# Kernel tuning notes

Measured on AMD Instinct MI355X. Metric: run time of the kernel, lower is better.

Reference implementation:

```python
import jax, jax.numpy as jnp
import numpy as np

T, D, F, E, K, R = 16384, 1024, 2048, 8, 2, 16
LORA_SCALING = 2.0


def setup_inputs() -> dict:
    key = jax.random.key(0)
    ks = jax.random.split(key, 9)
    s = 0.02
    return {
        "hidden_states": jax.random.normal(ks[0], (T, D), jnp.float32),
        "gate_weight": jax.random.normal(ks[1], (E, D), jnp.float32) * s,
        "gate_lora_delta": jax.random.normal(ks[2], (E, D), jnp.float32) * s,
        "gate_up_proj": jax.random.normal(ks[3], (E, D, 2 * F), jnp.float32) * s,
        "down_proj": jax.random.normal(ks[4], (E, F, D), jnp.float32) * s,
        "gu_lora_A": jax.random.normal(ks[5], (E, R, D), jnp.float32) * s,
        "gu_lora_B": jax.random.normal(ks[6], (E, 2 * F, R), jnp.float32) * s,
        "dn_lora_A": jax.random.normal(ks[7], (E, R, F), jnp.float32) * s,
        "dn_lora_B": jax.random.normal(ks[8], (E, D, R), jnp.float32) * s,
    }


def reference(hidden_states, gate_weight, gate_lora_delta, gate_up_proj,
              down_proj, gu_lora_A, gu_lora_B, dn_lora_A, dn_lora_B):
    x = hidden_states  # [T, D]
    # --- softmax top-k routing (base gate weight + LoRA delta) ---
    logits = x @ gate_weight.T + x @ gate_lora_delta.T            # [T, E]
    probs = jax.nn.softmax(logits.astype(jnp.float32), axis=-1)   # fp32 softmax
    topk_w, topk_idx = jax.lax.top_k(probs, K)                    # [T, K]
    topk_w = topk_w / jnp.sum(topk_w, axis=-1, keepdims=True)     # norm_topk_prob
    # dense combine weights [T, E]: 0 for unselected experts
    combine = jnp.zeros((x.shape[0], E), jnp.float32)
    combine = combine.at[jnp.arange(x.shape[0])[:, None], topk_idx].set(topk_w)
    # --- per-expert gated MLP with LoRA deltas, masked combine ---
    out = jnp.zeros_like(x, dtype=jnp.float32)
    for e in range(E):  # fixed small expert count
        gu = x @ gate_up_proj[e] + LORA_SCALING * ((x @ gu_lora_A[e].T) @ gu_lora_B[e].T)  # [T, 2F]
        gate, up = jnp.split(gu, 2, axis=-1)
        h = jax.nn.silu(gate) * up                                                        # [T, F]
        y = h @ down_proj[e] + LORA_SCALING * ((h @ dn_lora_A[e].T) @ dn_lora_B[e].T)     # [T, D]
        out = out + combine[:, e:e + 1] * y
    return out.astype(hidden_states.dtype)
```

## Files before the change

kernel.cpp:

```cpp
#include <hip/hip_runtime.h>
#include <stdint.h>

#define T_TOK 16384
#define DH    1024
#define FF    2048
#define NE    8
#define NC    4096
#define PADROWS 34816
#define BK    32

typedef __attribute__((ext_vector_type(8))) __bf16 bf16x8;
typedef __attribute__((ext_vector_type(4))) float  f32x4;

__device__ __forceinline__ float bf2f(unsigned short s) {
  unsigned int u = ((unsigned int)s) << 16;
  return __builtin_bit_cast(float, u);
}
__device__ __forceinline__ unsigned short f2bf(float f) {
  unsigned int u = __builtin_bit_cast(unsigned int, f);
  u += 0x7fffu + ((u >> 16) & 1u);
  return (unsigned short)(u >> 16);
}

__device__ __forceinline__ void gload_lds16(const void* g, void* l) {
  __builtin_amdgcn_global_load_lds(
      (__attribute__((address_space(1))) void*)(uintptr_t)g,
      (__attribute__((address_space(3))) void*)(uint32_t)(uintptr_t)l,
      16, 0, 0);
}

__device__ __forceinline__ int origc_gu(int c) {
  int g = c >> 5, wi = c & 31;
  return ((wi >> 4) << 11) | (g * 16 + (wi & 15));
}

__global__ __launch_bounds__(256) void fold_gu_kernel(
    const float* __restrict__ Wg, const float* __restrict__ A,
    const float* __restrict__ B, unsigned short* __restrict__ Wf)
{
  const int e = blockIdx.x, d0 = blockIdx.y * 64, c0 = blockIdx.z * 64;
  __shared__ float tile[64][65];
  __shared__ float Al[16][64];
  __shared__ float Bl[64][17];
  const int tid = threadIdx.x;
  {
    int r = tid >> 4, dc = (tid & 15) * 4;
    float4 v = *(const float4*)&A[((size_t)e * 16 + r) * DH + d0 + dc];
    Al[r][dc] = v.x; Al[r][dc + 1] = v.y; Al[r][dc + 2] = v.z; Al[r][dc + 3] = v.w;
  }
  {
    int c = tid >> 2, rr = (tid & 3) * 4;
    float4 v = *(const float4*)&B[((size_t)e * NC + origc_gu(c0 + c)) * 16 + rr];
    Bl[c][rr] = v.x; Bl[c][rr + 1] = v.y; Bl[c][rr + 2] = v.z; Bl[c][rr + 3] = v.w;
  }
  __syncthreads();
  const int d = tid >> 2;
  const int cq0 = (tid & 3) * 4;
  float areg[16];
#pragma unroll
  for (int r = 0; r < 16; r++) areg[r] = Al[r][d];
#pragma unroll
  for (int p = 0; p < 4; p++) {
    const int cq = p * 16 + cq0;
    float4 v = *(const float4*)&Wg[((size_t)e * DH + d0 + d) * NC + origc_gu(c0 + cq)];
    float s0 = 0.f, s1 = 0.f, s2 = 0.f, s3 = 0.f;
#pragma unroll
    for (int r = 0; r < 16; r++) {
      float a = areg[r];
      s0 += a * Bl[cq][r];     s1 += a * Bl[cq + 1][r];
      s2 += a * Bl[cq + 2][r]; s3 += a * Bl[cq + 3][r];
    }
    tile[d][cq]     = v.x + 2.f * s0; tile[d][cq + 1] = v.y + 2.f * s1;
    tile[d][cq + 2] = v.z + 2.f * s2; tile[d][cq + 3] = v.w + 2.f * s3;
  }
  __syncthreads();
#pragma unroll
  for (int p = 0; p < 2; p++) {
    int flat = p * 256 + tid;
    int c = flat >> 3, dch = (flat & 7) * 8;
    unsigned short u[8];
#pragma unroll
    for (int j = 0; j < 8; j++) u[j] = f2bf(tile[dch + j][c]);
    *(uint4*)&Wf[((size_t)e * NC + c0 + c) * DH + d0 + dch] = *(uint4*)u;
  }
}

__global__ __launch_bounds__(256) void fold_dn_kernel(
    const float* __restrict__ Wd, const float* __restrict__ A,
    const float* __restrict__ B, unsigned short* __restrict__ Wf)
{
  const int e = blockIdx.x, f0 = blockIdx.y * 64, d0 = blockIdx.z * 64;
  __shared__ float tile[64][65];
  __shared__ float Al[16][64];
  __shared__ float Bl[64][17];
  const int tid = threadIdx.x;
  {
    int r = tid >> 4, fc = (tid & 15) * 4;
    float4 v = *(const float4*)&A[((size_t)e * 16 + r) * FF + f0 + fc];
    Al[r][fc] = v.x; Al[r][fc + 1] = v.y; Al[r][fc + 2] = v.z; Al[r][fc + 3] = v.w;
  }
  {
    int d = tid >> 2, rr = (tid & 3) * 4;
    float4 v = *(const float4*)&B[((size_t)e * DH + d0 + d) * 16 + rr];
    Bl[d][rr] = v.x; Bl[d][rr + 1] = v.y; Bl[d][rr + 2] = v.z; Bl[d][rr + 3] = v.w;
  }
  __syncthreads();
  const int f = tid >> 2;
  const int dq0 = (tid & 3) * 4;
  float areg[16];
#pragma unroll
  for (int r = 0; r < 16; r++) areg[r] = Al[r][f];
#pragma unroll
  for (int p = 0; p < 4; p++) {
    const int dq = p * 16 + dq0;
    float4 v = *(const float4*)&Wd[((size_t)e * FF + f0 + f) * DH + d0 + dq];
    float s0 = 0.f, s1 = 0.f, s2 = 0.f, s3 = 0.f;
#pragma unroll
    for (int r = 0; r < 16; r++) {
      float a = areg[r];
      s0 += a * Bl[dq][r];     s1 += a * Bl[dq + 1][r];
      s2 += a * Bl[dq + 2][r]; s3 += a * Bl[dq + 3][r];
    }
    tile[f][dq]     = v.x + 2.f * s0; tile[f][dq + 1] = v.y + 2.f * s1;
    tile[f][dq + 2] = v.z + 2.f * s2; tile[f][dq + 3] = v.w + 2.f * s3;
  }
  __syncthreads();
#pragma unroll
  for (int p = 0; p < 2; p++) {
    int flat = p * 256 + tid;
    int d = flat >> 3, fch = (flat & 7) * 8;
    unsigned short u[8];
#pragma unroll
    for (int j = 0; j < 8; j++) u[j] = f2bf(tile[fch + j][d]);
    *(uint4*)&Wf[((size_t)e * DH + d0 + d) * FF + f0 + fch] = *(uint4*)u;
  }
}

__global__ __launch_bounds__(256) void route_kernel(
    const float* __restrict__ X,
    const float* __restrict__ GW,
    const float* __restrict__ GLD,
    unsigned short* __restrict__ Xbf,
    int* __restrict__ tokE, float* __restrict__ tokW, int* __restrict__ counts)
{
  __shared__ float gc[NE * DH];
  __shared__ int bc[NE];
  const int tid = threadIdx.x;
  if (tid < NE) bc[tid] = 0;
  for (int i = tid; i < NE * DH; i += 256) gc[i] = GW[i] + GLD[i];
  __syncthreads();
  const int w = tid >> 6, lane = tid & 63;
  for (int it = 0; it < 8; it++) {
    const int t = blockIdx.x * 32 + w * 8 + it;
    float s[NE];
#pragma unroll
    for (int e = 0; e < NE; e++) s[e] = 0.f;
#pragma unroll
    for (int i = 0; i < 8; i++) {
      const int base = 2 * lane + 128 * i;
      const float2 xv = *(const float2*)&X[(size_t)t * DH + base];
      *(unsigned*)&Xbf[(size_t)t * DH + base] =
          (unsigned)f2bf(xv.x) | ((unsigned)f2bf(xv.y) << 16);
#pragma unroll
      for (int e = 0; e < NE; e++) {
        float2 g2 = *(const float2*)&gc[e * DH + base];
        s[e] += xv.x * g2.x + xv.y * g2.y;
      }
    }
#pragma unroll
    for (int e = 0; e < NE; e++) {
#pragma unroll
      for (int off = 32; off > 0; off >>= 1) s[e] += __shfl_xor(s[e], off);
    }
    int e1 = 0; float l1 = s[0];
#pragma unroll
    for (int e = 1; e < NE; e++) { if (s[e] > l1) { l1 = s[e]; e1 = e; } }
    int e2i = 0; float l2 = -3.4e38f;
#pragma unroll
    for (int e = 0; e < NE; e++) { if (e != e1 && s[e] > l2) { l2 = s[e]; e2i = e; } }
    float r = __expf(l2 - l1);
    float w0 = 1.f / (1.f + r);
    if (lane == 0) {
      tokE[2 * t] = e1; tokE[2 * t + 1] = e2i;
      tokW[2 * t] = w0; tokW[2 * t + 1] = 1.f - w0;
      atomicAdd(&bc[e1], 1); atomicAdd(&bc[e2i], 1);
    }
  }
  __syncthreads();
  if (tid < NE) atomicAdd(&counts[tid], bc[tid]);
}

__global__ void offs_kernel(const int* __restrict__ counts, int* __restrict__ offs) {
  if (threadIdx.x == 0) {
    int run = 0;
#pragma unroll
    for (int e = 0; e < NE; e++) { offs[e] = run; run += (counts[e] + 255) & ~255; }
    offs[NE] = run;
  }
}

__global__ void scatter_kernel(const int* __restrict__ tokE,
                               const int* __restrict__ offs,
                               int* __restrict__ cursor,
                               int* __restrict__ posTok,
                               int* __restrict__ posOf)
{
  const int t = blockIdx.x * 256 + threadIdx.x;
  const int lane = threadIdx.x & 63;
#pragma unroll
  for (int k = 0; k < 2; k++) {
    const int e = tokE[2 * t + k];
    int p = 0;
#pragma unroll
    for (int ei = 0; ei < NE; ei++) {
      unsigned long long mask = __ballot(e == ei);
      if (mask) {
        int leader = __ffsll((unsigned long long)mask) - 1;
        int base = 0;
        if (lane == leader) base = atomicAdd(&cursor[ei], (int)__popcll(mask));
        base = __shfl(base, leader);
        if (e == ei)
          p = offs[ei] + base + (int)__popcll(mask & ((1ull << lane) - 1ull));
      }
    }
    if (p < 0) p = 0;
    if (p >= PADROWS) p = PADROWS - 1;
    posTok[p] = t;
    posOf[2 * t + k] = p;
  }
}


#define STAGE_A(s) { unsigned short* d_ = (unsigned short*)&lds[(s) & 3][0][w * 512]; \
  gload_lds16(gA0 + (size_t)(s) * BK, d_); gload_lds16(gA1 + (size_t)(s) * BK, d_ + 4096); }
#define STAGE_B(s) { unsigned short* d_ = (unsigned short*)&lds[(s) & 3][1][w * 512]; \
  gload_lds16(gB0 + (size_t)(s) * BK, d_); gload_lds16(gB1 + (size_t)(s) * BK, d_ + 4096); }

#define PHASE_MFMA(ACCROW, AV)                                              \
  __builtin_amdgcn_s_barrier();                                             \
  __builtin_amdgcn_s_setprio(1);                                            \
  _Pragma("unroll")                                                         \
  for (int mi = 0; mi < 4; mi++)                                            \
    _Pragma("unroll")                                                       \
    for (int ni = 0; ni < 4; ni++)                                          \
      acc[(ACCROW) + mi][ni] = __builtin_amdgcn_mfma_f32_16x16x32_bf16(     \
          AV[mi], b[ni], acc[(ACCROW) + mi][ni], 0, 0, 0);                  \
  __builtin_amdgcn_s_setprio(0);                                            \
  __builtin_amdgcn_s_barrier();

__global__ __launch_bounds__(512, 2) void gemm1_kernel(
    const unsigned short* __restrict__ Xbf,
    const unsigned short* __restrict__ Wgu,
    const int* __restrict__ posTok,
    const int* __restrict__ offs,
    unsigned short* __restrict__ H)
{
  __shared__ __align__(16) unsigned short lds[4][2][8192];
  const int NT = DH / BK;
  const int n0 = blockIdx.x * 256;
  const int row0 = blockIdx.y * 256;
  if (row0 >= offs[NE]) return;
  int e = 0;
#pragma unroll
  for (int i = 1; i < NE; i++) e += (row0 >= offs[i]) ? 1 : 0;
  const unsigned short* Wb = Wgu + (size_t)e * NC * DH;

  const int tid = threadIdx.x;
  const int lane = tid & 63;
  const int w = tid >> 6;
  const int wm = w >> 2, wn = w & 3;
  const int l15 = lane & 15, quad = lane >> 4;

  const int srow = tid >> 2;
  const int sch  = (tid & 3) ^ ((srow >> 1) & 3);
  int t0 = posTok[row0 + srow];       if (t0 < 0) t0 = 0;
  int t1 = posTok[row0 + 128 + srow]; if (t1 < 0) t1 = 0;
  const unsigned short* gA0 = Xbf + (size_t)t0 * DH + sch * 8;
  const unsigned short* gA1 = Xbf + (size_t)t1 * DH + sch * 8;
  const unsigned short* gB0 = Wb + (size_t)(n0 + srow) * DH + sch * 8;
  const unsigned short* gB1 = Wb + (size_t)(n0 + 128 + srow) * DH + sch * 8;

  const int slot  = quad ^ ((l15 >> 1) & 3);
  const int aBase = (wm * 128 + l15) * 32 + slot * 8;
  const int bBase = (wn * 64 + l15) * 32 + slot * 8;

  f32x4 acc[8][4];
#pragma unroll
  for (int mi = 0; mi < 8; mi++)
#pragma unroll
    for (int ni = 0; ni < 4; ni++) acc[mi][ni] = (f32x4){0.f, 0.f, 0.f, 0.f};

  STAGE_A(0); STAGE_B(0);
  STAGE_A(1); STAGE_B(1);
  STAGE_A(2); STAGE_B(2);
  asm volatile("s_waitcnt vmcnt(8)" ::: "memory");
  __builtin_amdgcn_s_barrier();

  for (int kt = 0; kt < NT; ++kt) {
    const unsigned short* LA = &lds[kt & 3][0][0];
    const unsigned short* LB = &lds[kt & 3][1][0];
    bf16x8 a[4], b[4];
#pragma unroll
    for (int i = 0; i < 4; i++) a[i] = *(const bf16x8*)&LA[aBase + i * 512];
#pragma unroll
    for (int i = 0; i < 4; i++) b[i] = *(const bf16x8*)&LB[bBase + i * 512];
    if (kt + 3 < NT) STAGE_A(kt + 3);
    PHASE_MFMA(0, a)
    bf16x8 a2[4];
#pragma unroll
    for (int i = 0; i < 4; i++) a2[i] = *(const bf16x8*)&LA[aBase + (4 + i) * 512];
    if (kt + 3 < NT) STAGE_B(kt + 3);
    if (kt + 3 < NT)       { asm volatile("s_waitcnt vmcnt(8)" ::: "memory"); }
    else if (kt + 3 == NT) { asm volatile("s_waitcnt vmcnt(4)" ::: "memory"); }
    else if (kt + 1 < NT)  { asm volatile("s_waitcnt vmcnt(0)" ::: "memory"); }
    PHASE_MFMA(4, a2)
  }

  const int rowb = row0 + wm * 128;
#pragma unroll
  for (int mi = 0; mi < 8; mi++) {
#pragma unroll
    for (int p = 0; p < 2; p++) {
      f32x4 g = acc[mi][2 * p], u = acc[mi][2 * p + 1];
      int f = (n0 >> 1) + wn * 32 + p * 16 + l15;
#pragma unroll
      for (int r = 0; r < 4; r++) {
        int row = rowb + mi * 16 + quad * 4 + r;
        float gv = g[r];
        float hv = (gv / (1.f + __expf(-gv))) * u[r];
        H[(size_t)row * FF + f] = f2bf(hv);
      }
    }
  }
}

__global__ __launch_bounds__(512, 2) void gemm2_kernel(
    const unsigned short* __restrict__ H,
    const unsigned short* __restrict__ Wdn,
    const int* __restrict__ offs,
    unsigned short* __restrict__ Y)
{
  __shared__ __align__(16) unsigned short lds[4][2][8192];
  const int NT = FF / BK;
  const int n0 = blockIdx.x * 256;
  const int row0 = blockIdx.y * 256;
  if (row0 >= offs[NE]) return;
  int e = 0;
#pragma unroll
  for (int i = 1; i < NE; i++) e += (row0 >= offs[i]) ? 1 : 0;
  const unsigned short* Wb = Wdn + (size_t)e * DH * FF;

  const int tid = threadIdx.x;
  const int lane = tid & 63;
  const int w = tid >> 6;
  const int wm = w >> 2, wn = w & 3;
  const int l15 = lane & 15, quad = lane >> 4;

  const int srow = tid >> 2;
  const int sch  = (tid & 3) ^ ((srow >> 1) & 3);
  const unsigned short* gA0 = H + (size_t)(row0 + srow) * FF + sch * 8;
  const unsigned short* gA1 = H + (size_t)(row0 + 128 + srow) * FF + sch * 8;
  const unsigned short* gB0 = Wb + (size_t)(n0 + srow) * FF + sch * 8;
  const unsigned short* gB1 = Wb + (size_t)(n0 + 128 + srow) * FF + sch * 8;

  const int slot  = quad ^ ((l15 >> 1) & 3);
  const int aBase = (wm * 128 + l15) * 32 + slot * 8;
  const int bBase = (wn * 64 + l15) * 32 + slot * 8;

  f32x4 acc[8][4];
#pragma unroll
  for (int mi = 0; mi < 8; mi++)
#pragma unroll
    for (int ni = 0; ni < 4; ni++) acc[mi][ni] = (f32x4){0.f, 0.f, 0.f, 0.f};

  STAGE_A(0); STAGE_B(0);
  STAGE_A(1); STAGE_B(1);
  STAGE_A(2); STAGE_B(2);
  asm volatile("s_waitcnt vmcnt(8)" ::: "memory");
  __builtin_amdgcn_s_barrier();

  for (int kt = 0; kt < NT; ++kt) {
    const unsigned short* LA = &lds[kt & 3][0][0];
    const unsigned short* LB = &lds[kt & 3][1][0];
    bf16x8 a[4], b[4];
#pragma unroll
    for (int i = 0; i < 4; i++) a[i] = *(const bf16x8*)&LA[aBase + i * 512];
#pragma unroll
    for (int i = 0; i < 4; i++) b[i] = *(const bf16x8*)&LB[bBase + i * 512];
    if (kt + 3 < NT) STAGE_A(kt + 3);
    PHASE_MFMA(0, a)
    bf16x8 a2[4];
#pragma unroll
    for (int i = 0; i < 4; i++) a2[i] = *(const bf16x8*)&LA[aBase + (4 + i) * 512];
    if (kt + 3 < NT) STAGE_B(kt + 3);
    if (kt + 3 < NT)       { asm volatile("s_waitcnt vmcnt(8)" ::: "memory"); }
    else if (kt + 3 == NT) { asm volatile("s_waitcnt vmcnt(4)" ::: "memory"); }
    else if (kt + 1 < NT)  { asm volatile("s_waitcnt vmcnt(0)" ::: "memory"); }
    PHASE_MFMA(4, a2)
  }

#pragma unroll
  for (int mi = 0; mi < 8; mi++)
#pragma unroll
    for (int ni = 0; ni < 4; ni++) {
      int col = n0 + wn * 64 + ni * 16 + l15;
#pragma unroll
      for (int r = 0; r < 4; r++) {
        int row = row0 + wm * 128 + mi * 16 + quad * 4 + r;
        Y[(size_t)row * DH + col] = f2bf(acc[mi][ni][r]);
      }
    }
}

__global__ void combine_kernel(const unsigned short* __restrict__ Y,
                               const int* __restrict__ posOf,
                               const float* __restrict__ tokW,
                               float* __restrict__ out)
{
  int idx = blockIdx.x * 256 + threadIdx.x;
  int t = idx >> 7;
  int c = (idx & 127) * 8;
  int p0 = posOf[2 * t], p1 = posOf[2 * t + 1];
  float w0 = tokW[2 * t], w1 = tokW[2 * t + 1];
  const uint4 a = *(const uint4*)&Y[(size_t)p0 * DH + c];
  const uint4 b = *(const uint4*)&Y[(size_t)p1 * DH + c];
  const unsigned* ap = (const unsigned*)&a;
  const unsigned* bp = (const unsigned*)&b;
  float4 o0, o1;
#pragma unroll
  for (int i = 0; i < 4; i++) {
    float a0 = bf2f((unsigned short)(ap[i] & 0xffff)), a1 = bf2f((unsigned short)(ap[i] >> 16));
    float b0 = bf2f((unsigned short)(bp[i] & 0xffff)), b1 = bf2f((unsigned short)(bp[i] >> 16));
    float r0 = w0 * a0 + w1 * b0;
    float r1 = w0 * a1 + w1 * b1;
    if (i < 2) { ((float*)&o0)[2 * i] = r0; ((float*)&o0)[2 * i + 1] = r1; }
    else       { ((float*)&o1)[2 * (i - 2)] = r0; ((float*)&o1)[2 * (i - 2) + 1] = r1; }
  }
  *(float4*)&out[(size_t)t * DH + c]     = o0;
  *(float4*)&out[(size_t)t * DH + c + 4] = o1;
}

extern "C" void kernel_launch(void* const* d_in, const int* in_sizes, int n_in,
                              void* d_out, int out_size, void* d_ws, size_t ws_size,
                              hipStream_t stream)
{
  const float* X   = (const float*)d_in[0];
  const float* GW  = (const float*)d_in[1];
  const float* GLD = (const float*)d_in[2];
  const float* GUP = (const float*)d_in[3];
  const float* DNP = (const float*)d_in[4];
  const float* GUA = (const float*)d_in[5];
  const float* GUB = (const float*)d_in[6];
  const float* DNA = (const float*)d_in[7];
  const float* DNB = (const float*)d_in[8];
  float* OUT = (float*)d_out;

  char* p = (char*)d_ws;
  unsigned short* Wguf = (unsigned short*)p; p += (size_t)NE * NC * DH * 2;
  unsigned short* Wdnf = (unsigned short*)p; p += (size_t)NE * DH * FF * 2;
  unsigned short* H    = (unsigned short*)p; p += (size_t)PADROWS * FF * 2;
  unsigned short* Y    = (unsigned short*)p; p += (size_t)PADROWS * DH * 2;
  int*   posTok = (int*)p;   p += (size_t)PADROWS * 4;
  int*   posOf  = (int*)p;   p += (size_t)T_TOK * 2 * 4;
  int*   tokE   = (int*)p;   p += (size_t)T_TOK * 2 * 4;
  float* tokW   = (float*)p; p += (size_t)T_TOK * 2 * 4;
  int*   counts = (int*)p;   p += 32;
  int*   cursor = (int*)p;   p += 32;
  int*   offs   = (int*)p;   p += 64;
  if ((size_t)(p - (char*)d_ws) > ws_size) return;

  unsigned short* Xbf = Y;

  hipMemsetAsync(counts, 0, 32 + 32 + 64, stream);
  hipMemsetAsync(posTok, 0xFF, (size_t)PADROWS * 4, stream);

  fold_gu_kernel<<<dim3(NE, DH / 64, NC / 64), 256, 0, stream>>>(GUP, GUA, GUB, Wguf);
  fold_dn_kernel<<<dim3(NE, FF / 64, DH / 64), 256, 0, stream>>>(DNP, DNA, DNB, Wdnf);
  route_kernel<<<T_TOK / 32, 256, 0, stream>>>(X, GW, GLD, Xbf, tokE, tokW, counts);
  offs_kernel<<<1, 64, 0, stream>>>(counts, offs);
  scatter_kernel<<<T_TOK / 256, 256, 0, stream>>>(tokE, offs, cursor, posTok, posOf);
  gemm1_kernel<<<dim3(NC / 256, PADROWS / 256), 512, 0, stream>>>(Xbf, Wguf, posTok, offs, H);
  gemm2_kernel<<<dim3(DH / 256, PADROWS / 256), 512, 0, stream>>>(H, Wdnf, offs, Y);
  combine_kernel<<<(T_TOK * DH / 8) / 256, 256, 0, stream>>>(Y, posOf, tokW, OUT);
}
```

Measured before the change: 925.4 us.

## Halve gemm2 row tile to 128 and swizzle block order in both GEMMs

gemm2 now uses 128-row by 256-col tiles with separate A and B LDS buffers and a single MFMA phase per k-step, doubling the grid rows so more blocks are in flight (gemm2 has only 4 column tiles). Both gemm1 and gemm2 remap the linear block id so that consecutive blocks, likely spread across XCDs, share weight column tiles and row ranges, aiming for better L2 reuse. The smaller tile lowers arithmetic intensity and re-reads weights more often, and the per-k-step barrier adds sync overhead.

Result: slower. 944.0 us (+2.0%).

```diff
diff --git a/kernel.cpp b/kernel.cpp
--- a/kernel.cpp
+++ b/kernel.cpp
@@ -8,6 +8,8 @@
 #define NC    4096
 #define PADROWS 34816
 #define BK    32
+#define NROW256 136
+#define NROW128 272
 
 typedef __attribute__((ext_vector_type(8))) __bf16 bf16x8;
 typedef __attribute__((ext_vector_type(4))) float  f32x4;
@@ -257,8 +259,10 @@
 {
   __shared__ __align__(16) unsigned short lds[4][2][8192];
   const int NT = DH / BK;
-  const int n0 = blockIdx.x * 256;
-  const int row0 = blockIdx.y * 256;
+  const int lin = blockIdx.y * gridDim.x + blockIdx.x;
+  const int swz = (lin & 7) * (2 * NROW256) + (lin >> 3);
+  const int n0   = (swz / NROW256) * 256;
+  const int row0 = (swz % NROW256) * 256;
   if (row0 >= offs[NE]) return;
   int e = 0;
 #pragma unroll
@@ -334,16 +338,24 @@
   }
 }
 
+#define G2STAGE_A(s) { unsigned short* d_ = &ldsA[(s) & 3][w * 512]; \
+  gload_lds16(gA0 + (size_t)(s) * BK, d_); }
+#define G2STAGE_B(s) { unsigned short* d_ = &ldsB[(s) & 3][w * 512]; \
+  gload_lds16(gB0 + (size_t)(s) * BK, d_); gload_lds16(gB1 + (size_t)(s) * BK, d_ + 4096); }
+
 __global__ __launch_bounds__(512, 2) void gemm2_kernel(
     const unsigned short* __restrict__ H,
     const unsigned short* __restrict__ Wdn,
     const int* __restrict__ offs,
     unsigned short* __restrict__ Y)
 {
-  __shared__ __align__(16) unsigned short lds[4][2][8192];
+  __shared__ __align__(16) unsigned short ldsA[4][4096];
+  __shared__ __align__(16) unsigned short ldsB[4][8192];
   const int NT = FF / BK;
-  const int n0 = blockIdx.x * 256;
-  const int row0 = blockIdx.y * 256;
+  const int lin = blockIdx.y * gridDim.x + blockIdx.x;
+  const int swz = (lin & 7) * (NROW128 / 2) + (lin >> 3);
+  const int n0   = (swz / NROW128) * 256;
+  const int row0 = (swz % NROW128) * 128;
   if (row0 >= offs[NE]) return;
   int e = 0;
 #pragma unroll
@@ -359,54 +371,56 @@
   const int srow = tid >> 2;
   const int sch  = (tid & 3) ^ ((srow >> 1) & 3);
   const unsigned short* gA0 = H + (size_t)(row0 + srow) * FF + sch * 8;
-  const unsigned short* gA1 = H + (size_t)(row0 + 128 + srow) * FF + sch * 8;
   const unsigned short* gB0 = Wb + (size_t)(n0 + srow) * FF + sch * 8;
   const unsigned short* gB1 = Wb + (size_t)(n0 + 128 + srow) * FF + sch * 8;
 
   const int slot  = quad ^ ((l15 >> 1) & 3);
-  const int aBase = (wm * 128 + l15) * 32 + slot * 8;
+  const int aBase = (wm * 64 + l15) * 32 + slot * 8;
   const int bBase = (wn * 64 + l15) * 32 + slot * 8;
 
-  f32x4 acc[8][4];
-#pragma unroll
-  for (int mi = 0; mi < 8; mi++)
+  f32x4 acc[4][4];
+#pragma unroll
+  for (int mi = 0; mi < 4; mi++)
 #pragma unroll
     for (int ni = 0; ni < 4; ni++) acc[mi][ni] = (f32x4){0.f, 0.f, 0.f, 0.f};
 
-  STAGE_A(0); STAGE_B(0);
-  STAGE_A(1); STAGE_B(1);
-  STAGE_A(2); STAGE_B(2);
-  asm volatile("s_waitcnt vmcnt(8)" ::: "memory");
+  G2STAGE_A(0); G2STAGE_B(0);
+  G2STAGE_A(1); G2STAGE_B(1);
+  G2STAGE_A(2); G2STAGE_B(2);
+  asm volatile("s_waitcnt vmcnt(6)" ::: "memory");
   __builtin_amdgcn_s_barrier();
 
   for (int kt = 0; kt < NT; ++kt) {
-    const unsigned short* LA = &lds[kt & 3][0][0];
-    const unsigned short* LB = &lds[kt & 3][1][0];
+    const unsigned short* LA = &ldsA[kt & 3][0];
+    const unsigned short* LB = &ldsB[kt & 3][0];
     bf16x8 a[4], b[4];
 #pragma unroll
     for (int i = 0; i < 4; i++) a[i] = *(const bf16x8*)&LA[aBase + i * 512];
 #pragma unroll
     for (int i = 0; i < 4; i++) b[i] = *(const bf16x8*)&LB[bBase + i * 512];
-    if (kt + 3 < NT) STAGE_A(kt + 3);
-    PHASE_MFMA(0, a)
-    bf16x8 a2[4];
-#pragma unroll
-    for (int i = 0; i < 4; i++) a2[i] = *(const bf16x8*)&LA[aBase + (4 + i) * 512];
-    if (kt + 3 < NT) STAGE_B(kt + 3);
-    if (kt + 3 < NT)       { asm volatile("s_waitcnt vmcnt(8)" ::: "memory"); }
-    else if (kt + 3 == NT) { asm volatile("s_waitcnt vmcnt(4)" ::: "memory"); }
+    if (kt + 3 < NT) { G2STAGE_A(kt + 3); G2STAGE_B(kt + 3); }
+    if (kt + 3 < NT)       { asm volatile("s_waitcnt vmcnt(6)" ::: "memory"); }
+    else if (kt + 3 == NT) { asm volatile("s_waitcnt vmcnt(3)" ::: "memory"); }
     else if (kt + 1 < NT)  { asm volatile("s_waitcnt vmcnt(0)" ::: "memory"); }
-    PHASE_MFMA(4, a2)
-  }
-
-#pragma unroll
-  for (int mi = 0; mi < 8; mi++)
+    __builtin_amdgcn_s_barrier();
+    __builtin_amdgcn_s_setprio(1);
+#pragma unroll
+    for (int mi = 0; mi < 4; mi++)
+#pragma unroll
+      for (int ni = 0; ni < 4; ni++)
+        acc[mi][ni] = __builtin_amdgcn_mfma_f32_16x16x32_bf16(a[mi], b[ni], acc[mi][ni], 0, 0, 0);
+    __builtin_amdgcn_s_setprio(0);
+    __builtin_amdgcn_s_barrier();
+  }
+
+#pragma unroll
+  for (int mi = 0; mi < 4; mi++)
 #pragma unroll
     for (int ni = 0; ni < 4; ni++) {
       int col = n0 + wn * 64 + ni * 16 + l15;
 #pragma unroll
       for (int r = 0; r < 4; r++) {
-        int row = row0 + wm * 128 + mi * 16 + quad * 4 + r;
+        int row = row0 + wm * 64 + mi * 16 + quad * 4 + r;
         Y[(size_t)row * DH + col] = f2bf(acc[mi][ni][r]);
       }
     }
@@ -480,6 +494,6 @@
   offs_kernel<<<1, 64, 0, stream>>>(counts, offs);
   scatter_kernel<<<T_TOK / 256, 256, 0, stream>>>(tokE, offs, cursor, posTok, posOf);
   gemm1_kernel<<<dim3(NC / 256, PADROWS / 256), 512, 0, stream>>>(Xbf, Wguf, posTok, offs, H);
-  gemm2_kernel<<<dim3(DH / 256, PADROWS / 256), 512, 0, stream>>>(H, Wdnf, offs, Y);
+  gemm2_kernel<<<dim3(DH / 256, PADROWS / 128), 512, 0, stream>>>(H, Wdnf, offs, Y);
   combine_kernel<<<(T_TOK * DH / 8) / 256, 256, 0, stream>>>(Y, posOf, tokW, OUT);
 }
```

## Split grouped GEMM launches into row chunks and add small-tile gemm2 tail kernel

Applied to the files above, without the earlier changes.

Adds a rowBase parameter so gemm1 runs as five launches over row chunks instead of one large grid, and gemm2 covers the first 32768 rows with the existing 256-row-tile kernel. A new gemm2_tail_kernel with 128-row tiles covers the last 2048 padded rows, so the final partial tiles are spread over more blocks. The aim is to cut wave-quantization and tail idle time, and to raise gemm1 locality by processing rows chunk by chunk. The cost is extra launch overhead and more code to maintain.

Result: no change. 927.4 us (+0.2%).

```diff
diff --git a/kernel.cpp b/kernel.cpp
--- a/kernel.cpp
+++ b/kernel.cpp
@@ -253,12 +253,13 @@
     const unsigned short* __restrict__ Wgu,
     const int* __restrict__ posTok,
     const int* __restrict__ offs,
-    unsigned short* __restrict__ H)
+    unsigned short* __restrict__ H,
+    int rowBase)
 {
   __shared__ __align__(16) unsigned short lds[4][2][8192];
   const int NT = DH / BK;
   const int n0 = blockIdx.x * 256;
-  const int row0 = blockIdx.y * 256;
+  const int row0 = rowBase + blockIdx.y * 256;
   if (row0 >= offs[NE]) return;
   int e = 0;
 #pragma unroll
@@ -338,12 +339,13 @@
     const unsigned short* __restrict__ H,
     const unsigned short* __restrict__ Wdn,
     const int* __restrict__ offs,
-    unsigned short* __restrict__ Y)
+    unsigned short* __restrict__ Y,
+    int rowBase)
 {
   __shared__ __align__(16) unsigned short lds[4][2][8192];
   const int NT = FF / BK;
   const int n0 = blockIdx.x * 256;
-  const int row0 = blockIdx.y * 256;
+  const int row0 = rowBase + blockIdx.y * 256;
   if (row0 >= offs[NE]) return;
   int e = 0;
 #pragma unroll
@@ -407,6 +409,93 @@
 #pragma unroll
       for (int r = 0; r < 4; r++) {
         int row = row0 + wm * 128 + mi * 16 + quad * 4 + r;
+        Y[(size_t)row * DH + col] = f2bf(acc[mi][ni][r]);
+      }
+    }
+}
+
+#define G2STAGE_A(s) { unsigned short* d_ = &ldsA[(s) & 3][w * 512]; \
+  gload_lds16(gA0 + (size_t)(s) * BK, d_); }
+#define G2STAGE_B(s) { unsigned short* d_ = &ldsB[(s) & 3][w * 512]; \
+  gload_lds16(gB0 + (size_t)(s) * BK, d_); gload_lds16(gB1 + (size_t)(s) * BK, d_ + 4096); }
+
+__global__ __launch_bounds__(512, 2) void gemm2_tail_kernel(
+    const unsigned short* __restrict__ H,
+    const unsigned short* __restrict__ Wdn,
+    const int* __restrict__ offs,
+    unsigned short* __restrict__ Y,
+    int rowBase)
+{
+  __shared__ __align__(16) unsigned short ldsA[4][4096];
+  __shared__ __align__(16) unsigned short ldsB[4][8192];
+  const int NT = FF / BK;
+  const int n0 = blockIdx.x * 256;
+  const int row0 = rowBase + blockIdx.y * 128;
+  if (row0 >= offs[NE]) return;
+  int e = 0;
+#pragma unroll
+  for (int i = 1; i < NE; i++) e += (row0 >= offs[i]) ? 1 : 0;
+  const unsigned short* Wb = Wdn + (size_t)e * DH * FF;
+
+  const int tid = threadIdx.x;
+  const int lane = tid & 63;
+  const int w = tid >> 6;
+  const int wm = w >> 2, wn = w & 3;
+  const int l15 = lane & 15, quad = lane >> 4;
+
+  const int srow = tid >> 2;
+  const int sch  = (tid & 3) ^ ((srow >> 1) & 3);
+  const unsigned short* gA0 = H + (size_t)(row0 + srow) * FF + sch * 8;
+  const unsigned short* gB0 = Wb + (size_t)(n0 + srow) * FF + sch * 8;
+  const unsigned short* gB1 = Wb + (size_t)(n0 + 128 + srow) * FF + sch * 8;
+
+  const int slot  = quad ^ ((l15 >> 1) & 3);
+  const int aBase = (wm * 64 + l15) * 32 + slot * 8;
+  const int bBase = (wn * 64 + l15) * 32 + slot * 8;
+
+  f32x4 acc[4][4];
+#pragma unroll
+  for (int mi = 0; mi < 4; mi++)
+#pragma unroll
+    for (int ni = 0; ni < 4; ni++) acc[mi][ni] = (f32x4){0.f, 0.f, 0.f, 0.f};
+
+  G2STAGE_A(0); G2STAGE_B(0);
+  G2STAGE_A(1); G2STAGE_B(1);
+  G2STAGE_A(2); G2STAGE_B(2);
+  asm volatile("s_waitcnt vmcnt(6)" ::: "memory");
+  __builtin_amdgcn_s_barrier();
+
+  for (int kt = 0; kt < NT; ++kt) {
+    const unsigned short* LA = &ldsA[kt & 3][0];
+    const unsigned short* LB = &ldsB[kt & 3][0];
+    bf16x8 a[4], b[4];
+#pragma unroll
+    for (int i = 0; i < 4; i++) a[i] = *(const bf16x8*)&LA[aBase + i * 512];
+#pragma unroll
+    for (int i = 0; i < 4; i++) b[i] = *(const bf16x8*)&LB[bBase + i * 512];
+    if (kt + 3 < NT) { G2STAGE_A(kt + 3); G2STAGE_B(kt + 3); }
+    if (kt + 3 < NT)       { asm volatile("s_waitcnt vmcnt(6)" ::: "memory"); }
+    else if (kt + 3 == NT) { asm volatile("s_waitcnt vmcnt(3)" ::: "memory"); }
+    else if (kt + 1 < NT)  { asm volatile("s_waitcnt vmcnt(0)" ::: "memory"); }
+    __builtin_amdgcn_s_barrier();
+    __builtin_amdgcn_s_setprio(1);
+#pragma unroll
+    for (int mi = 0; mi < 4; mi++)
+#pragma unroll
+      for (int ni = 0; ni < 4; ni++)
+        acc[mi][ni] = __builtin_amdgcn_mfma_f32_16x16x32_bf16(a[mi], b[ni], acc[mi][ni], 0, 0, 0);
+    __builtin_amdgcn_s_setprio(0);
+    __builtin_amdgcn_s_barrier();
+  }
+
+#pragma unroll
+  for (int mi = 0; mi < 4; mi++)
+#pragma unroll
+    for (int ni = 0; ni < 4; ni++) {
+      int col = n0 + wn * 64 + ni * 16 + l15;
+#pragma unroll
+      for (int r = 0; r < 4; r++) {
+        int row = row0 + wm * 64 + mi * 16 + quad * 4 + r;
         Y[(size_t)row * DH + col] = f2bf(acc[mi][ni][r]);
       }
     }
@@ -479,7 +568,15 @@
   route_kernel<<<T_TOK / 32, 256, 0, stream>>>(X, GW, GLD, Xbf, tokE, tokW, counts);
   offs_kernel<<<1, 64, 0, stream>>>(counts, offs);
   scatter_kernel<<<T_TOK / 256, 256, 0, stream>>>(tokE, offs, cursor, posTok, posOf);
-  gemm1_kernel<<<dim3(NC / 256, PADROWS / 256), 512, 0, stream>>>(Xbf, Wguf, posTok, offs, H);
-  gemm2_kernel<<<dim3(DH / 256, PADROWS / 256), 512, 0, stream>>>(H, Wdnf, offs, Y);
+
+  gemm1_kernel<<<dim3(16, 32), 512, 0, stream>>>(Xbf, Wguf, posTok, offs, H, 0);
+  gemm1_kernel<<<dim3(16, 32), 512, 0, stream>>>(Xbf, Wguf, posTok, offs, H, 8192);
+  gemm1_kernel<<<dim3(16, 32), 512, 0, stream>>>(Xbf, Wguf, posTok, offs, H, 16384);
+  gemm1_kernel<<<dim3(16, 32), 512, 0, stream>>>(Xbf, Wguf, posTok, offs, H, 24576);
+  gemm1_kernel<<<dim3(16, 8),  512, 0, stream>>>(Xbf, Wguf, posTok, offs, H, 32768);
+
+  gemm2_kernel<<<dim3(4, 128), 512, 0, stream>>>(H, Wdnf, offs, Y, 0);
+  gemm2_tail_kernel<<<dim3(4, 16), 512, 0, stream>>>(H, Wdnf, offs, Y, 32768);
+
   combine_kernel<<<(T_TOK * DH / 8) / 256, 256, 0, stream>>>(Y, posOf, tokW, OUT);
 }
```
